# Kernel tuning notes

Hardware: AMD Instinct MI355X
Metric: run time of the kernel (lower is better)

The kernel has to match this reference:

```python
import jax, jax.numpy as jnp
import numpy as np

NUM_HEADS = 16
HIDDEN = 1024
HEAD_DIM = HIDDEN // NUM_HEADS
BS, SEQ = 2, 2048


def setup_inputs() -> dict:
    key = jax.random.key(0)
    ks = jax.random.split(key, 9)
    s = 1.0 / np.sqrt(HIDDEN)
    return {
        "Q": jax.random.normal(ks[0], (BS, SEQ, HIDDEN), jnp.float32),
        "K": jax.random.normal(ks[1], (BS, SEQ, HIDDEN), jnp.float32),
        "V": jax.random.normal(ks[2], (BS, SEQ, HIDDEN), jnp.float32),
        "attention_mask": jnp.zeros((BS, 1, 1, SEQ), jnp.float32),
        # nn.Linear weights stored as [in, out] (already transposed)
        "Wq": jax.random.uniform(ks[3], (HIDDEN, HIDDEN), jnp.float32, -s, s),
        "bq": jax.random.uniform(ks[4], (HIDDEN,), jnp.float32, -s, s),
        "Wk": jax.random.uniform(ks[5], (HIDDEN, HIDDEN), jnp.float32, -s, s),
        "bk": jax.random.uniform(ks[6], (HIDDEN,), jnp.float32, -s, s),
        "Wv": jax.random.uniform(ks[7], (HIDDEN, HIDDEN), jnp.float32, -s, s),
        "bv": jax.random.uniform(ks[8], (HIDDEN,), jnp.float32, -s, s),
    }


def _split_heads(x):
    b, s, _ = x.shape
    return x.reshape(b, s, NUM_HEADS, HEAD_DIM).transpose(0, 2, 1, 3)  # [b,h,s,d]


def reference(Q, K, V, attention_mask, Wq, bq, Wk, bk, Wv, bv):
    q = _split_heads(Q @ Wq + bq)  # [b,h,s,d]
    k = _split_heads(K @ Wk + bk)
    v = _split_heads(V @ Wv + bv)
    score = jnp.einsum("bhqd,bhkd->bhqk", q, k)
    # NOTE: original adds mask BEFORE scaling by 1/sqrt(d)
    score = (score + attention_mask) / np.sqrt(HEAD_DIM)
    attn = jax.nn.softmax(score, axis=-1)
    out = jnp.einsum("bhqk,bhkd->bqhd", attn, v)  # [b,q,h,d]
    b, s = Q.shape[:2]
    return out.reshape(b, s, NUM_HEADS * HEAD_DIM)
```

## Files before the change

kernel.cpp:

```cpp
#include <hip/hip_runtime.h>
#include <hip/hip_bf16.h>
#include <stdint.h>

#define SEQ    2048
#define HIDDEN 1024
#define NH     16
#define HD     64

#define SC_LOG2E_8 0.18033688011112042f
#define SM_SHIFT   16.0f

typedef __bf16 bf16x8 __attribute__((ext_vector_type(8)));
typedef float  f32x4  __attribute__((ext_vector_type(4)));
typedef float  f32x16 __attribute__((ext_vector_type(16)));
typedef unsigned int uint32x2 __attribute__((ext_vector_type(2)));

typedef __attribute__((address_space(1))) void* as1vp;
typedef __attribute__((address_space(3))) void* as3vp;

__device__ __forceinline__ void gload_lds16(const void* g, void* l) {
  __builtin_amdgcn_global_load_lds((as1vp)(void*)g, (as3vp)l, 16, 0, 0);
}

__device__ __forceinline__ uint16_t f2bf(float f) {
  uint32_t x;
  __builtin_memcpy(&x, &f, 4);
  x += 0x7FFFu + ((x >> 16) & 1u);
  return (uint16_t)(x >> 16);
}

__device__ __forceinline__ uint32_t pkbf(float lo, float hi) {
  union { __bf16 v[2]; uint32_t u; } t;
  t.v[0] = (__bf16)lo; t.v[1] = (__bf16)hi;
  return t.u;
}

__device__ __forceinline__ uint32x2 plswap(uint32_t lo, uint32_t hi) {
  return __builtin_amdgcn_permlane32_swap(lo, hi, false, false);
}

__device__ __forceinline__ float xhalf32(float x, int lane) {
  uint32_t a;
  __builtin_memcpy(&a, &x, 4);
  uint32x2 r = plswap(a, a);
  uint32_t p = (lane < 32) ? r[1] : r[0];
  float f;
  __builtin_memcpy(&f, &p, 4);
  return f;
}

__device__ __forceinline__ float exp2_fast(float x) {
  return __builtin_amdgcn_exp2f(x);
}

__global__ __launch_bounds__(256) void k_cvt(
    const float* __restrict__ Q, const float* __restrict__ K, const float* __restrict__ V,
    const float* __restrict__ mask,
    uint16_t* __restrict__ Qb, uint16_t* __restrict__ Kb, uint16_t* __restrict__ Vb,
    float* __restrict__ mask_sc) {
  if (blockIdx.x == 2048) {
    if (blockIdx.y < 2) {
      const int i = (blockIdx.y * 256 + threadIdx.x) * 8;
      float4 a = *(const float4*)(mask + i);
      float4 b = *(const float4*)(mask + i + 4);
      a.x = a.x * SC_LOG2E_8 - SM_SHIFT; a.y = a.y * SC_LOG2E_8 - SM_SHIFT;
      a.z = a.z * SC_LOG2E_8 - SM_SHIFT; a.w = a.w * SC_LOG2E_8 - SM_SHIFT;
      b.x = b.x * SC_LOG2E_8 - SM_SHIFT; b.y = b.y * SC_LOG2E_8 - SM_SHIFT;
      b.z = b.z * SC_LOG2E_8 - SM_SHIFT; b.w = b.w * SC_LOG2E_8 - SM_SHIFT;
      *(float4*)(mask_sc + i) = a;
      *(float4*)(mask_sc + i + 4) = b;
    }
    return;
  }
  const float* src = (blockIdx.y == 0) ? Q : (blockIdx.y == 1) ? K : V;
  uint16_t*    dst = (blockIdx.y == 0) ? Qb : (blockIdx.y == 1) ? Kb : Vb;
  const int i = (blockIdx.x * 256 + threadIdx.x) * 8;
  float4 v0 = *(const float4*)(src + i);
  float4 v1 = *(const float4*)(src + i + 4);
  uint16_t tmp[8];
  tmp[0] = f2bf(v0.x); tmp[1] = f2bf(v0.y); tmp[2] = f2bf(v0.z); tmp[3] = f2bf(v0.w);
  tmp[4] = f2bf(v1.x); tmp[5] = f2bf(v1.y); tmp[6] = f2bf(v1.z); tmp[7] = f2bf(v1.w);
  __builtin_memcpy(dst + i, tmp, 16);
}

__global__ __launch_bounds__(256) void k_transpose(
    const float* __restrict__ W0, const float* __restrict__ W1, const float* __restrict__ W2,
    uint16_t* __restrict__ T0, uint16_t* __restrict__ T1, uint16_t* __restrict__ T2) {
  __shared__ uint16_t t[64][65];
  const float* W = (blockIdx.y == 0) ? W0 : (blockIdx.y == 1) ? W1 : W2;
  uint16_t*    T = (blockIdx.y == 0) ? T0 : (blockIdx.y == 1) ? T1 : T2;
  const int bx = blockIdx.x & 15, by = blockIdx.x >> 4;
  const int tx = threadIdx.x & 63, ty = threadIdx.x >> 6;
  for (int i = ty; i < 64; i += 4)
    t[i][tx] = f2bf(W[(by * 64 + i) * HIDDEN + bx * 64 + tx]);
  __syncthreads();
  for (int i = ty; i < 64; i += 4)
    T[(bx * 64 + i) * HIDDEN + by * 64 + tx] = t[tx][i];
}

__global__ __launch_bounds__(256) void k_qkv_gemm(
    const uint16_t* __restrict__ Qb, const uint16_t* __restrict__ Kb, const uint16_t* __restrict__ Vb,
    const uint16_t* __restrict__ WTq, const uint16_t* __restrict__ WTk, const uint16_t* __restrict__ WTv,
    const float* __restrict__ Bq, const float* __restrict__ Bk, const float* __restrict__ Bv,
    uint16_t* __restrict__ q_ws, uint16_t* __restrict__ k_ws, uint16_t* __restrict__ v_ws) {
  const int wg  = blockIdx.x;
  const int swz = (wg & 7) * 96 + (wg >> 3);
  const int mode = swz >> 8;
  const int rem  = swz & 255;
  const int m0   = (rem >> 3) * 128;
  const int n0   = (rem & 7) * 128;

  const uint16_t* X   = (mode == 0) ? Qb : (mode == 1) ? Kb : Vb;
  const uint16_t* WT  = (mode == 0) ? WTq : (mode == 1) ? WTk : WTv;
  const float*    bia = (mode == 0) ? Bq  : (mode == 1) ? Bk  : Bv;

  __shared__ uint16_t As[128 * 64];
  __shared__ uint16_t Bs[128 * 64];
  char* AsB = (char*)As;
  char* BsB = (char*)Bs;

  const int tid  = threadIdx.x;
  const int lane = tid & 63;
  const int w    = tid >> 6;
  const int wr   = w >> 1, wc = w & 1;

  const int lrow = lane >> 3;
  const int lcol = (lane & 7) * 16;

  f32x4 acc[4][4];
  const f32x4 zero = {0.f, 0.f, 0.f, 0.f};
#pragma unroll
  for (int i = 0; i < 4; ++i)
#pragma unroll
    for (int j = 0; j < 4; ++j) acc[i][j] = zero;

  const char* Ab = (const char*)X;
  const char* Bb = (const char*)WT;

  for (int kt = 0; kt < 16; ++kt) {
    __syncthreads();
    const int kbyte = kt * 128;
#pragma unroll
    for (int i = 0; i < 4; ++i) {
      const int r = w * 32 + i * 8;
      gload_lds16(Ab + (size_t)(m0 + r + lrow) * (HIDDEN * 2) + kbyte + lcol, AsB + r * 128);
      gload_lds16(Bb + (size_t)(n0 + r + lrow) * (HIDDEN * 2) + kbyte + lcol, BsB + r * 128);
    }
    __syncthreads();
#pragma unroll
    for (int kc = 0; kc < 2; ++kc) {
      const int chunk = kc * 64 + (lane >> 4) * 16;
      bf16x8 a[4], b[4];
#pragma unroll
      for (int f = 0; f < 4; ++f) {
        const int ra = wr * 64 + f * 16 + (lane & 15);
        a[f] = *(const bf16x8*)(AsB + ra * 128 + chunk);
        const int rb = wc * 64 + f * 16 + (lane & 15);
        b[f] = *(const bf16x8*)(BsB + rb * 128 + chunk);
      }
#pragma unroll
      for (int fm = 0; fm < 4; ++fm)
#pragma unroll
        for (int fn = 0; fn < 4; ++fn)
          acc[fm][fn] = __builtin_amdgcn_mfma_f32_16x16x32_bf16(a[fm], b[fn], acc[fm][fn], 0, 0, 0);
    }
  }

  float bfrag[4];
#pragma unroll
  for (int fn = 0; fn < 4; ++fn)
    bfrag[fn] = bia[n0 + wc * 64 + fn * 16 + (lane & 15)];

#pragma unroll
  for (int fm = 0; fm < 4; ++fm) {
    const int mrow0 = m0 + wr * 64 + fm * 16 + (lane >> 4) * 4;
    const int b0 = mrow0 >> 11;
    const int sq = mrow0 & (SEQ - 1);
#pragma unroll
    for (int fn = 0; fn < 4; ++fn) {
      const int n = n0 + wc * 64 + fn * 16 + (lane & 15);
      const int h = n >> 6, d = n & 63;
      const size_t bh = (size_t)(b0 * NH + h);
      if (mode == 2) {
        const int kt2 = sq >> 6, ks = (sq >> 4) & 3, hv = (sq >> 3) & 1, jj = sq & 7;
        const int dt = d >> 5, lnv = hv * 32 + (d & 31);
        uint16_t tmp[4];
#pragma unroll
        for (int j = 0; j < 4; ++j) tmp[j] = f2bf(acc[fm][fn][j] + bfrag[fn]);
        __builtin_memcpy(v_ws + ((((bh * 32 + kt2) * 2 + dt) * 4 + ks) * 64 + lnv) * 8 + jj,
                         tmp, 8);
      } else if (mode == 1) {
        const int kt2 = sq >> 6, c = (sq >> 5) & 1, ql = sq & 31;
        const int slot = d >> 4, hk = (d >> 3) & 1, jk = d & 7;
        uint16_t* base = k_ws + ((((bh * 32 + kt2) * 2 + c) * 4 + slot) * 64 + hk * 32 + ql) * 8 + jk;
#pragma unroll
        for (int j = 0; j < 4; ++j) base[j * 8] = f2bf(acc[fm][fn][j] + bfrag[fn]);
      } else {
        const int qt32 = sq >> 5, ql = sq & 31;
        const int slot = d >> 4, hq = (d >> 3) & 1, jq = d & 7;
        uint16_t* base = q_ws + (((bh * 64 + qt32) * 4 + slot) * 64 + hq * 32 + ql) * 8 + jq;
#pragma unroll
        for (int j = 0; j < 4; ++j)
          base[j * 8] = f2bf((acc[fm][fn][j] + bfrag[fn]) * SC_LOG2E_8);
      }
    }
  }
}

__global__ __launch_bounds__(256) void k_attn(
    const uint16_t* __restrict__ q_ws, const uint16_t* __restrict__ k_ws,
    const uint16_t* __restrict__ v_ws, const float* __restrict__ mask_sc,
    float* __restrict__ out) {
  __shared__ float smem[3][64][33];

  const int tid = threadIdx.x, lane = tid & 63, w = tid >> 6;
  const int wg  = blockIdx.x;
  const int swz = (wg & 7) * 256 + (wg >> 3);
  const int bh  = swz >> 6;
  const int qt  = swz & 63;
  const int b   = bh >> 4;
  const int h   = bh & 15;
  const int q0  = qt * 32;
  const int ql  = lane & 31;
  const int hi  = lane >> 5;

  const char* qfb = (const char*)q_ws + ((size_t)bh * 64 + qt) * 4096;
  const char* kfb = (const char*)k_ws + (size_t)bh * 262144 + lane * 16;
  const char* vfb = (const char*)v_ws + (size_t)bh * 262144 + lane * 16;
  const float* mrow = mask_sc + b * SEQ;

  bf16x8 qB[4];
#pragma unroll
  for (int s = 0; s < 4; ++s)
    qB[s] = *(const bf16x8*)(qfb + s * 1024 + lane * 16);

  const f32x16 zero16 = {0.f};
  f32x16 Oacc[2];
  Oacc[0] = zero16; Oacc[1] = zero16;
  float lpart = 0.f;

  const int kbeg = w * 8, kend = kbeg + 8;

  for (int kt = kbeg; kt < kend; ++kt) {
    const char* kt_k = kfb + (size_t)kt * 8192;
    const char* kt_v = vfb + (size_t)kt * 8192;

    bf16x8 kf[8];
#pragma unroll
    for (int i = 0; i < 8; ++i) kf[i] = *(const bf16x8*)(kt_k + i * 1024);

    f32x16 P0, P1;
#pragma unroll
    for (int g = 0; g < 4; ++g) {
      f32x4 mk0 = *(const f32x4*)(mrow + kt * 64 + g * 8 + 4 * hi);
      f32x4 mk1 = *(const f32x4*)(mrow + kt * 64 + 32 + g * 8 + 4 * hi);
#pragma unroll
      for (int t = 0; t < 4; ++t) { P0[g * 4 + t] = mk0[t]; P1[g * 4 + t] = mk1[t]; }
    }

#pragma unroll
    for (int s = 0; s < 4; ++s)
      P0 = __builtin_amdgcn_mfma_f32_32x32x16_bf16(kf[s], qB[s], P0, 0, 0, 0);
#pragma unroll
    for (int s = 0; s < 4; ++s)
      P1 = __builtin_amdgcn_mfma_f32_32x32x16_bf16(kf[4 + s], qB[s], P1, 0, 0, 0);

    bf16x8 vA[8];
#pragma unroll
    for (int i = 0; i < 8; ++i) vA[i] = *(const bf16x8*)(kt_v + i * 1024);

    float s0 = 0.f, s1 = 0.f, s2a = 0.f, s3 = 0.f;
#pragma unroll
    for (int r = 0; r < 16; r += 4) {
      P0[r]     = exp2_fast(P0[r]);      s0  += P0[r];
      P0[r + 1] = exp2_fast(P0[r + 1]);  s1  += P0[r + 1];
      P0[r + 2] = exp2_fast(P0[r + 2]);  s2a += P0[r + 2];
      P0[r + 3] = exp2_fast(P0[r + 3]);  s3  += P0[r + 3];
      P1[r]     = exp2_fast(P1[r]);      s0  += P1[r];
      P1[r + 1] = exp2_fast(P1[r + 1]);  s1  += P1[r + 1];
      P1[r + 2] = exp2_fast(P1[r + 2]);  s2a += P1[r + 2];
      P1[r + 3] = exp2_fast(P1[r + 3]);  s3  += P1[r + 3];
    }
    lpart += (s0 + s1) + (s2a + s3);

    bf16x8 pb[4];
#pragma unroll
    for (int ks = 0; ks < 4; ++ks) {
      const int o = (ks & 1) * 8;
      uint32_t w0, w1, w2, w3;
      if (ks < 2) {
        w0 = pkbf(P0[o + 0], P0[o + 1]);
        w1 = pkbf(P0[o + 2], P0[o + 3]);
        w2 = pkbf(P0[o + 4], P0[o + 5]);
        w3 = pkbf(P0[o + 6], P0[o + 7]);
      } else {
        w0 = pkbf(P1[o + 0], P1[o + 1]);
        w1 = pkbf(P1[o + 2], P1[o + 3]);
        w2 = pkbf(P1[o + 4], P1[o + 5]);
        w3 = pkbf(P1[o + 6], P1[o + 7]);
      }
      uint32x2 r02 = plswap(w0, w2);
      uint32x2 r13 = plswap(w1, w3);
      uint32_t wv[4] = {r02[0], r13[0], r02[1], r13[1]};
      __builtin_memcpy(&pb[ks], wv, 16);
    }

#pragma unroll
    for (int ks = 0; ks < 4; ++ks) {
      Oacc[0] = __builtin_amdgcn_mfma_f32_32x32x16_bf16(vA[ks],     pb[ks], Oacc[0], 0, 0, 0);
      Oacc[1] = __builtin_amdgcn_mfma_f32_32x32x16_bf16(vA[4 + ks], pb[ks], Oacc[1], 0, 0, 0);
    }
  }

  if (w > 0) {
    float* s = smem[w - 1][lane];
#pragma unroll
    for (int r = 0; r < 16; ++r) { s[r] = Oacc[0][r]; s[16 + r] = Oacc[1][r]; }
    s[32] = lpart;
  }
  __syncthreads();
  if (w > 0) return;

#pragma unroll
  for (int p = 0; p < 3; ++p) {
    const float* s = smem[p][lane];
#pragma unroll
    for (int r = 0; r < 16; ++r) { Oacc[0][r] += s[r]; Oacc[1][r] += s[16 + r]; }
    lpart += s[32];
  }

  const float ltot = lpart + xhalf32(lpart, lane);
  const float linv = 1.f / ltot;
  float* orow = out + ((size_t)(b * SEQ) + q0 + ql) * HIDDEN + h * HD;
#pragma unroll
  for (int dt = 0; dt < 2; ++dt)
#pragma unroll
    for (int g = 0; g < 4; ++g) {
      f32x4 o;
#pragma unroll
      for (int t = 0; t < 4; ++t) o[t] = Oacc[dt][g * 4 + t] * linv;
      *(f32x4*)(orow + dt * 32 + g * 8 + 4 * hi) = o;
    }
}

extern "C" void kernel_launch(void* const* d_in, const int* in_sizes, int n_in,
                              void* d_out, int out_size, void* d_ws, size_t ws_size,
                              hipStream_t stream) {
  (void)in_sizes; (void)n_in; (void)out_size; (void)ws_size;
  const float* Q    = (const float*)d_in[0];
  const float* K    = (const float*)d_in[1];
  const float* V    = (const float*)d_in[2];
  const float* mask = (const float*)d_in[3];
  const float* Wq   = (const float*)d_in[4];
  const float* bq   = (const float*)d_in[5];
  const float* Wk   = (const float*)d_in[6];
  const float* bk   = (const float*)d_in[7];
  const float* Wv   = (const float*)d_in[8];
  const float* bv   = (const float*)d_in[9];

  uint16_t* ws   = (uint16_t*)d_ws;
  uint16_t* wt_q = ws;
  uint16_t* wt_k = wt_q + HIDDEN * HIDDEN;
  uint16_t* wt_v = wt_k + HIDDEN * HIDDEN;
  const size_t qkv = (size_t)2 * SEQ * HIDDEN;
  uint16_t* Qb   = wt_v + HIDDEN * HIDDEN;
  uint16_t* Kb   = Qb + qkv;
  uint16_t* Vb   = Kb + qkv;
  uint16_t* q_ws = Vb + qkv;
  uint16_t* k_ws = q_ws + qkv;
  uint16_t* v_ws = k_ws + qkv;
  float* mask_sc = (float*)(v_ws + qkv);

  k_cvt<<<dim3(2049, 3), 256, 0, stream>>>(Q, K, V, mask, Qb, Kb, Vb, mask_sc);
  k_transpose<<<dim3(256, 3), 256, 0, stream>>>(Wq, Wk, Wv, wt_q, wt_k, wt_v);
  k_qkv_gemm<<<dim3(768), 256, 0, stream>>>(
      Qb, Kb, Vb, wt_q, wt_k, wt_v, bq, bk, bv, q_ws, k_ws, v_ws);
  k_attn<<<dim3(2048), 256, 0, stream>>>(q_ws, k_ws, v_ws, mask_sc,
                                         (float*)d_out);
}
```

Before: 133.3 us.

## Merge prep kernels, double-buffer K loads in attention, add occupancy hint

Folds the weight transpose/convert kernel into the input-conversion kernel so one launch does both. In the attention kernel, K fragments for the next tile are loaded while the current tile is computed, using two ping-pong register buffers. It also adds a launch-bounds minimum of two blocks per SM. The prefetch raises register pressure, which the occupancy hint may force into spills, and the merged prep kernel now reserves shared memory in every block.

```diff
diff --git a/kernel.cpp b/kernel.cpp
--- a/kernel.cpp
+++ b/kernel.cpp
@@ -53,11 +53,27 @@
   return __builtin_amdgcn_exp2f(x);
 }
 
-__global__ __launch_bounds__(256) void k_cvt(
+__global__ __launch_bounds__(256) void k_prep(
     const float* __restrict__ Q, const float* __restrict__ K, const float* __restrict__ V,
     const float* __restrict__ mask,
+    const float* __restrict__ W0, const float* __restrict__ W1, const float* __restrict__ W2,
     uint16_t* __restrict__ Qb, uint16_t* __restrict__ Kb, uint16_t* __restrict__ Vb,
-    float* __restrict__ mask_sc) {
+    float* __restrict__ mask_sc,
+    uint16_t* __restrict__ T0, uint16_t* __restrict__ T1, uint16_t* __restrict__ T2) {
+  __shared__ uint16_t t[64][65];
+  if (blockIdx.x > 2048) {
+    const int bi = blockIdx.x - 2049;
+    const float* W = (blockIdx.y == 0) ? W0 : (blockIdx.y == 1) ? W1 : W2;
+    uint16_t*    T = (blockIdx.y == 0) ? T0 : (blockIdx.y == 1) ? T1 : T2;
+    const int bx = bi & 15, by = bi >> 4;
+    const int tx = threadIdx.x & 63, ty = threadIdx.x >> 6;
+    for (int i = ty; i < 64; i += 4)
+      t[i][tx] = f2bf(W[(by * 64 + i) * HIDDEN + bx * 64 + tx]);
+    __syncthreads();
+    for (int i = ty; i < 64; i += 4)
+      T[(bx * 64 + i) * HIDDEN + by * 64 + tx] = t[tx][i];
+    return;
+  }
   if (blockIdx.x == 2048) {
     if (blockIdx.y < 2) {
       const int i = (blockIdx.y * 256 + threadIdx.x) * 8;
@@ -83,21 +99,6 @@
   __builtin_memcpy(dst + i, tmp, 16);
 }
 
-__global__ __launch_bounds__(256) void k_transpose(
-    const float* __restrict__ W0, const float* __restrict__ W1, const float* __restrict__ W2,
-    uint16_t* __restrict__ T0, uint16_t* __restrict__ T1, uint16_t* __restrict__ T2) {
-  __shared__ uint16_t t[64][65];
-  const float* W = (blockIdx.y == 0) ? W0 : (blockIdx.y == 1) ? W1 : W2;
-  uint16_t*    T = (blockIdx.y == 0) ? T0 : (blockIdx.y == 1) ? T1 : T2;
-  const int bx = blockIdx.x & 15, by = blockIdx.x >> 4;
-  const int tx = threadIdx.x & 63, ty = threadIdx.x >> 6;
-  for (int i = ty; i < 64; i += 4)
-    t[i][tx] = f2bf(W[(by * 64 + i) * HIDDEN + bx * 64 + tx]);
-  __syncthreads();
-  for (int i = ty; i < 64; i += 4)
-    T[(bx * 64 + i) * HIDDEN + by * 64 + tx] = t[tx][i];
-}
-
 __global__ __launch_bounds__(256) void k_qkv_gemm(
     const uint16_t* __restrict__ Qb, const uint16_t* __restrict__ Kb, const uint16_t* __restrict__ Vb,
     const uint16_t* __restrict__ WTq, const uint16_t* __restrict__ WTk, const uint16_t* __restrict__ WTv,
@@ -207,7 +208,7 @@
   }
 }
 
-__global__ __launch_bounds__(256) void k_attn(
+__global__ __launch_bounds__(256, 2) void k_attn(
     const uint16_t* __restrict__ q_ws, const uint16_t* __restrict__ k_ws,
     const uint16_t* __restrict__ v_ws, const float* __restrict__ mask_sc,
     float* __restrict__ out) {
@@ -241,13 +242,20 @@
 
   const int kbeg = w * 8, kend = kbeg + 8;
 
-  for (int kt = kbeg; kt < kend; ++kt) {
-    const char* kt_k = kfb + (size_t)kt * 8192;
+  auto loadK = [&](int kt, bf16x8 (&kf)[8]) {
+    const char* p = kfb + (size_t)kt * 8192;
+#pragma unroll
+    for (int i = 0; i < 8; ++i) kf[i] = *(const bf16x8*)(p + i * 1024);
+  };
+
+  bf16x8 kA[8], kB[8];
+  loadK(kbeg, kA);
+
+  auto body = [&](int kt, bf16x8 (&kf)[8], bf16x8 (&kn)[8]) {
+    const int ktn = (kt + 1 < kend) ? kt + 1 : kend - 1;
+    loadK(ktn, kn);
+
     const char* kt_v = vfb + (size_t)kt * 8192;
-
-    bf16x8 kf[8];
-#pragma unroll
-    for (int i = 0; i < 8; ++i) kf[i] = *(const bf16x8*)(kt_k + i * 1024);
 
     f32x16 P0, P1;
 #pragma unroll
@@ -310,6 +318,11 @@
       Oacc[0] = __builtin_amdgcn_mfma_f32_32x32x16_bf16(vA[ks],     pb[ks], Oacc[0], 0, 0, 0);
       Oacc[1] = __builtin_amdgcn_mfma_f32_32x32x16_bf16(vA[4 + ks], pb[ks], Oacc[1], 0, 0, 0);
     }
+  };
+
+  for (int kt = kbeg; kt < kend; kt += 2) {
+    body(kt,     kA, kB);
+    body(kt + 1, kB, kA);
   }
 
   if (w > 0) {
@@ -371,8 +384,9 @@
   uint16_t* v_ws = k_ws + qkv;
   float* mask_sc = (float*)(v_ws + qkv);
 
-  k_cvt<<<dim3(2049, 3), 256, 0, stream>>>(Q, K, V, mask, Qb, Kb, Vb, mask_sc);
-  k_transpose<<<dim3(256, 3), 256, 0, stream>>>(Wq, Wk, Wv, wt_q, wt_k, wt_v);
+  k_prep<<<dim3(2305, 3), 256, 0, stream>>>(Q, K, V, mask, Wq, Wk, Wv,
+                                            Qb, Kb, Vb, mask_sc,
+                                            wt_q, wt_k, wt_v);
   k_qkv_gemm<<<dim3(768), 256, 0, stream>>>(
       Qb, Kb, Vb, wt_q, wt_k, wt_v, bq, bk, bv, q_ws, k_ws, v_ws);
   k_attn<<<dim3(2048), 256, 0, stream>>>(q_ws, k_ws, v_ws, mask_sc,
```

Measured after the change: 166.1 us. 24.7% more time.
